# Kernel optimization log

Hardware: AMD Instinct MI355X
Metric: run time of the kernel (lower is better)

## Reference

```python
import jax, jax.numpy as jnp
import numpy as np

B, S, D = 4, 2048, 1024
NH = 16
H2 = NH // 2
F = D // NH  # per-head hidden = 64
EXP = 4
DECAY_CONST = S // 512  # 4
EPS = 1e-5


def setup_inputs() -> dict:
    key = jax.random.key(0)
    ks = jax.random.split(key, 8)
    inp = {
        "x": jax.random.normal(ks[0], (B, S, D), dtype=jnp.float32),
        # token_norm / channel_norm params (LayerNorm init: ones/zeros)
        "g1": jnp.ones((D,), jnp.float32), "b1": jnp.zeros((D,), jnp.float32),
        "g2": jnp.ones((D,), jnp.float32), "b2": jnp.zeros((D,), jnp.float32),
        # per-head input projections [NH, D, F] and output projection
        "Wp": jax.random.normal(ks[1], (NH, D, F), jnp.float32) * 0.02,
        "bp": jnp.zeros((NH, F), jnp.float32),
        "Wo": jax.random.normal(ks[2], (D, D), jnp.float32) * 0.02,
        "bo": jnp.zeros((D,), jnp.float32),
        # ColRepeatCausalLinear: weight = 0.4, bias = 3 ; RowRepeat: -0.3, 0.2
        "w_col": jnp.full((H2, S), 0.4, jnp.float32),
        "b_col": jnp.full((H2, S), 3.0, jnp.float32),
        "w_row": jnp.full((H2, S), -0.3, jnp.float32),
        "b_row": jnp.full((H2, S), 0.2, jnp.float32),
        # decay_value params (ones, clipped to [0.9, 1] then ** (1/decay_constant))
        "dcol": jnp.ones((H2,), jnp.float32),
        "drow": jnp.ones((H2,), jnp.float32),
        # channel MLP
        "W1": jax.random.normal(ks[3], (D, EXP * D), jnp.float32) * 0.02,
        "c1": jnp.zeros((EXP * D,), jnp.float32),
        "W2": jax.random.normal(ks[4], (EXP * D, D), jnp.float32) * 0.02,
        "c2": jnp.zeros((D,), jnp.float32),
    }
    return inp


def _ln(x, g, b):
    m = jnp.mean(x, axis=-1, keepdims=True)
    v = jnp.mean(jnp.square(x - m), axis=-1, keepdims=True)
    return (x - m) * jax.lax.rsqrt(v + EPS) * g + b


def _forward(x, g1, b1, g2, b2, Wp, bp, Wo, bo, w_col, b_col, w_row, b_row,
             dcol, drow, W1, c1, W2, c2):
    decay_c = jnp.clip(dcol, 0.9, 1.0) ** (1.0 / DECAY_CONST)  # [H2]
    decay_r = jnp.clip(drow, 0.9, 1.0) ** (1.0 / DECAY_CONST)  # [H2]

    def step(carry, inp):
        cc, rc = carry                      # each [B, H2, F]
        xt, wc, bc, wr, br = inp            # xt [B, D]; wc/bc/wr/br [H2]
        # token mixing branch
        h = _ln(xt, g1, b1)
        proj = jnp.einsum('bd,hdf->bhf', h, Wp) + bp  # [B, NH, F]
        # Col heads: cache = proj + decay*cache ; out = w*cache + b
        cc = proj[:, :H2] + decay_c[None, :, None] * cc
        col_out = wc[None, :, None] * cc + bc[None, :, None]
        # Row heads: cache = w*proj + decay*cache ; out = cache + b
        rc = wr[None, :, None] * proj[:, H2:] + decay_r[None, :, None] * rc
        row_out = rc + br[None, :, None]
        mix = jnp.concatenate([col_out, row_out], axis=1).reshape(xt.shape[0], -1)
        y = xt + mix @ Wo + bo
        # channel MLP branch
        h2 = _ln(y, g2, b2)
        out = y + jax.nn.gelu(h2 @ W1 + c1) @ W2 + c2
        return (cc, rc), out

    init = (jnp.zeros((x.shape[0], H2, F), x.dtype),
            jnp.zeros((x.shape[0], H2, F), x.dtype))
    xs = (jnp.swapaxes(x, 0, 1), w_col.T, b_col.T, w_row.T, b_row.T)
    _, ys = jax.lax.scan(step, init, xs)    # ys [S, B, D]
    return jnp.swapaxes(ys, 0, 1)


def reference(x, g1, b1, g2, b2, Wp, bp, Wo, bo, w_col, b_col, w_row, b_row,
              dcol, drow, W1, c1, W2, c2):
    return _forward(x, g1, b1, g2, b2, Wp, bp, Wo, bo, w_col, b_col,
                    w_row, b_row, dcol, drow, W1, c1, W2, c2)
```

## Files before the change

### kernel.cpp

```cpp
#include <hip/hip_runtime.h>

typedef __attribute__((ext_vector_type(4))) float fx4;
typedef __attribute__((ext_vector_type(8))) short s16x8;

#define SEQ   2048
#define DM    1024
#define BSZ   4
#define ROWS  (BSZ*SEQ)
#define CHUNK 64
#define NCH   (SEQ/CHUNK)

__device__ __forceinline__ unsigned short f2bf(float f){
  unsigned u = __builtin_bit_cast(unsigned, f);
  u = u + 0x7FFFu + ((u >> 16) & 1u);
  return (unsigned short)(u >> 16);
}

__device__ __forceinline__ float gelu_f(float x){
  float u = 0.7978845608028654f * (x + 0.044715f * x*x*x);
  return x / (1.0f + __expf(-2.0f*u));
}

__device__ __forceinline__ void gload_lds16(const void* g, void* l){
  __builtin_amdgcn_global_load_lds(
      (__attribute__((address_space(1))) void*)g,
      (__attribute__((address_space(3))) void*)l, 16, 0, 0);
}

__global__ __launch_bounds__(256) void transpose_k(const float* __restrict__ in,
    unsigned short* __restrict__ out, int R, int C, long long ibs, long long obs){
  __shared__ float tile[32][33];
  in  += (long long)blockIdx.z * ibs;
  out += (long long)blockIdx.z * obs;
  int c0 = blockIdx.x*32, r0 = blockIdx.y*32;
  int tx = threadIdx.x, ty = threadIdx.y;
  #pragma unroll
  for (int i=0;i<4;i++)
    tile[ty+8*i][tx] = in[(long long)(r0+ty+8*i)*C + c0+tx];
  __syncthreads();
  #pragma unroll
  for (int i=0;i<4;i++)
    out[(long long)(c0+ty+8*i)*R + r0+tx] = f2bf(tile[tx][ty+8*i]);
}

__global__ __launch_bounds__(256) void ln_rows(const float* __restrict__ x,
    const float* __restrict__ g, const float* __restrict__ b,
    unsigned short* __restrict__ out){
  int row = blockIdx.x, t = threadIdx.x;
  const fx4* xr = (const fx4*)(x + (long long)row*DM);
  fx4 v = xr[t];
  float s  = v[0]+v[1]+v[2]+v[3];
  float s2 = v[0]*v[0]+v[1]*v[1]+v[2]*v[2]+v[3]*v[3];
  #pragma unroll
  for (int o=32;o;o>>=1){ s += __shfl_down(s,o); s2 += __shfl_down(s2,o); }
  __shared__ float red[8];
  int lane = t & 63, wid = t >> 6;
  if (lane==0){ red[wid]=s; red[4+wid]=s2; }
  __syncthreads();
  s  = red[0]+red[1]+red[2]+red[3];
  s2 = red[4]+red[5]+red[6]+red[7];
  float m  = s * (1.0f/DM);
  float rs = rsqrtf(s2*(1.0f/DM) - m*m + 1e-5f);
  const fx4 gv = ((const fx4*)g)[t], bv = ((const fx4*)b)[t];
  ushort4 pk;
  pk.x = f2bf((v[0]-m)*rs*gv[0] + bv[0]);
  pk.y = f2bf((v[1]-m)*rs*gv[1] + bv[1]);
  pk.z = f2bf((v[2]-m)*rs*gv[2] + bv[2]);
  pk.w = f2bf((v[3]-m)*rs*gv[3] + bv[3]);
  *(ushort4*)(out + (long long)row*DM + t*4) = pk;
}

__global__ __launch_bounds__(256) void scan_carry(const float* __restrict__ P,
    const float* __restrict__ w_row, const float* __restrict__ dcol,
    const float* __restrict__ drow, float* __restrict__ carry){
  int g = blockIdx.x*4 + (threadIdx.x>>6);
  int lane = threadIdx.x & 63;
  int chunk = g & (NCH-1); int bh = g >> 5; int h = bh & 15; int b = bh >> 4;
  float draw = (h<8) ? dcol[h] : drow[h-8];
  float d = powf(fminf(fmaxf(draw,0.9f),1.0f), 0.25f);
  float c = 0.f;
  const float* p = P + ((long long)(b*SEQ + chunk*CHUNK))*DM + h*64 + lane;
  const float* wr = w_row + (h>=8 ? (h-8)*SEQ + chunk*CHUNK : 0);
  #pragma unroll 4
  for (int i=0;i<CHUNK;i++){
    float a = p[(long long)i*DM];
    if (h>=8) a *= wr[i];
    c = fmaf(d, c, a);
  }
  carry[((long long)(bh*64 + lane))*NCH + chunk] = c;
}

__global__ __launch_bounds__(256) void scan_final(const float* __restrict__ P,
    const float* __restrict__ w_col, const float* __restrict__ b_col,
    const float* __restrict__ w_row, const float* __restrict__ b_row,
    const float* __restrict__ dcol, const float* __restrict__ drow,
    const float* __restrict__ carry, unsigned short* __restrict__ mix){
  int g = blockIdx.x*4 + (threadIdx.x>>6);
  int lane = threadIdx.x & 63;
  int chunk = g & (NCH-1); int bh = g >> 5; int h = bh & 15; int b = bh >> 4;
  float draw = (h<8) ? dcol[h] : drow[h-8];
  float d = powf(fminf(fmaxf(draw,0.9f),1.0f), 0.25f);
  float dL = d;
  #pragma unroll
  for (int i=0;i<6;i++) dL *= dL;
  const float* cr = carry + ((long long)(bh*64 + lane))*NCH;
  float c = 0.f;
  for (int j=0;j<chunk;j++) c = fmaf(dL, c, cr[j]);
  const float* p = P + ((long long)(b*SEQ + chunk*CHUNK))*DM + h*64 + lane;
  unsigned short* mo = mix + ((long long)(b*SEQ + chunk*CHUNK))*DM + h*64 + lane;
  int t0 = chunk*CHUNK;
  #pragma unroll 4
  for (int i=0;i<CHUNK;i++){
    int t = t0 + i;
    float a = p[(long long)i*DM];
    float o;
    if (h<8){
      c = fmaf(d, c, a);
      o = w_col[h*SEQ + t]*c + b_col[h*SEQ + t];
    } else {
      a *= w_row[(h-8)*SEQ + t];
      c = fmaf(d, c, a);
      o = c + b_row[(h-8)*SEQ + t];
    }
    mo[(long long)i*DM] = f2bf(o);
  }
}

template<int EPI, int K>
__global__ __launch_bounds__(256) void gemm_bt(const unsigned short* __restrict__ A,
    const unsigned short* __restrict__ Bt, int N,
    const float* __restrict__ bias, const float* __restrict__ res,
    float* __restrict__ outf, unsigned short* __restrict__ outb){
  __shared__ __align__(16) unsigned short lds[32768];
  const int tid = threadIdx.x;
  const int l = tid & 63;
  const int w = tid >> 6;
  const int wr = w >> 1, wc = w & 1;

  const long long row0 = (long long)blockIdx.x * 128;
  const long long col0 = (long long)blockIdx.y * 128;

  fx4 acc[4][4] = {};

  const unsigned short* gA[4];
  const unsigned short* gB[4];
  int lslot[4];
  #pragma unroll
  for (int i=0;i<4;i++){
    int slot = w*256 + i*64 + l;
    int r = slot >> 3;
    int qs = slot & 7;
    int c = (qs ^ (r & 7)) << 3;
    gA[i] = A  + (row0 + r)*(long long)K + c;
    gB[i] = Bt + (col0 + r)*(long long)K + c;
    lslot[i] = slot*8;
  }
  int aoff[2][4], boff[2][4];
  #pragma unroll
  for (int kk=0;kk<2;kk++){
    #pragma unroll
    for (int m=0;m<4;m++){
      int r  = wr*64 + m*16 + (l&15);
      int q  = (kk*4 + (l>>4)) ^ (r&7);
      aoff[kk][m] = r*64 + q*8;
      int r2 = wc*64 + m*16 + (l&15);
      int q2 = (kk*4 + (l>>4)) ^ (r2&7);
      boff[kk][m] = 8192 + r2*64 + q2*8;
    }
  }

  constexpr int nsteps = K >> 6;

  #pragma unroll
  for (int i=0;i<4;i++){
    gload_lds16(gA[i], &lds[lslot[i]]);
    gload_lds16(gB[i], &lds[8192 + lslot[i]]);
    gA[i] += 64; gB[i] += 64;
  }
  __syncthreads();

  int curoff = 0;
  for (int s = 0; s < nsteps-1; ++s){
    int nxt = curoff ^ 16384;
    #pragma unroll
    for (int i=0;i<4;i++){
      gload_lds16(gA[i], &lds[nxt + lslot[i]]);
      gload_lds16(gB[i], &lds[nxt + 8192 + lslot[i]]);
      gA[i] += 64; gB[i] += 64;
    }
    __builtin_amdgcn_s_setprio(1);
    #pragma unroll
    for (int kk=0;kk<2;kk++){
      s16x8 af[4], bfr[4];
      #pragma unroll
      for (int m=0;m<4;m++) af[m]  = *(const s16x8*)&lds[curoff + aoff[kk][m]];
      #pragma unroll
      for (int n=0;n<4;n++) bfr[n] = *(const s16x8*)&lds[curoff + boff[kk][n]];
      #pragma unroll
      for (int m=0;m<4;m++)
        #pragma unroll
        for (int n=0;n<4;n++)
          acc[m][n] = __builtin_amdgcn_mfma_f32_16x16x32_bf16(af[m], bfr[n], acc[m][n], 0, 0, 0);
    }
    __builtin_amdgcn_s_setprio(0);
    __syncthreads();
    curoff = nxt;
  }
  __builtin_amdgcn_s_setprio(1);
  #pragma unroll
  for (int kk=0;kk<2;kk++){
    s16x8 af[4], bfr[4];
    #pragma unroll
    for (int m=0;m<4;m++) af[m]  = *(const s16x8*)&lds[curoff + aoff[kk][m]];
    #pragma unroll
    for (int n=0;n<4;n++) bfr[n] = *(const s16x8*)&lds[curoff + boff[kk][n]];
    #pragma unroll
    for (int m=0;m<4;m++)
      #pragma unroll
      for (int n=0;n<4;n++)
        acc[m][n] = __builtin_amdgcn_mfma_f32_16x16x32_bf16(af[m], bfr[n], acc[m][n], 0, 0, 0);
  }
  __builtin_amdgcn_s_setprio(0);
  __syncthreads();

  float* lf = (float*)lds;
  const int lg = l >> 4, lc = l & 15;
  #pragma unroll
  for (int g=0; g<4; ++g){
    if (wr == (g>>1)){
      #pragma unroll
      for (int mm=0; mm<2; ++mm){
        const int m = (g&1)*2 + mm;
        int lrow = mm*16 + lg*4;
        #pragma unroll
        for (int n=0;n<4;n++){
          int col = wc*64 + n*16 + lc;
          #pragma unroll
          for (int rg=0;rg<4;rg++)
            lf[(lrow+rg)*132 + col] = acc[m][n][rg];
        }
      }
    }
    __syncthreads();
    #pragma unroll
    for (int j=0;j<4;j++){
      int flat = j*256 + tid;
      int lrow = flat >> 5, c4 = flat & 31;
      long long grow = row0 + g*32 + lrow;
      long long gcol = col0 + c4*4;
      fx4 v = *(fx4*)&lf[lrow*132 + c4*4];
      fx4 bv = *(const fx4*)&bias[gcol];
      v = v + bv;
      long long idx = grow*(long long)N + gcol;
      if constexpr (EPI==0){
        *(fx4*)&outf[idx] = v;
      } else if constexpr (EPI==1){
        fx4 rv = *(const fx4*)&res[idx];
        v = v + rv;
        *(fx4*)&outf[idx] = v;
      } else {
        ushort4 pk;
        pk.x = f2bf(gelu_f(v[0]));
        pk.y = f2bf(gelu_f(v[1]));
        pk.z = f2bf(gelu_f(v[2]));
        pk.w = f2bf(gelu_f(v[3]));
        *(ushort4*)&outb[idx] = pk;
      }
    }
    __syncthreads();
  }
}

extern "C" void kernel_launch(void* const* d_in, const int* in_sizes, int n_in,
                              void* d_out, int out_size, void* d_ws, size_t ws_size,
                              hipStream_t stream){
  const float* x    = (const float*)d_in[0];
  const float* g1   = (const float*)d_in[1];
  const float* b1   = (const float*)d_in[2];
  const float* g2   = (const float*)d_in[3];
  const float* b2   = (const float*)d_in[4];
  const float* Wp   = (const float*)d_in[5];
  const float* bp   = (const float*)d_in[6];
  const float* Wo   = (const float*)d_in[7];
  const float* bo   = (const float*)d_in[8];
  const float* w_col= (const float*)d_in[9];
  const float* b_col= (const float*)d_in[10];
  const float* w_row= (const float*)d_in[11];
  const float* b_row= (const float*)d_in[12];
  const float* dcol = (const float*)d_in[13];
  const float* drow = (const float*)d_in[14];
  const float* W1   = (const float*)d_in[15];
  const float* c1   = (const float*)d_in[16];
  const float* W2   = (const float*)d_in[17];
  const float* c2   = (const float*)d_in[18];
  float* out = (float*)d_out;

  char* ws = (char*)d_ws;
  const size_t MB = 1024*1024;
  if (ws_size < 101*MB) return;
  unsigned short* Wpt = (unsigned short*)(ws + 0);
  unsigned short* Wot = (unsigned short*)(ws + 2*MB);
  unsigned short* W1t = (unsigned short*)(ws + 4*MB);
  unsigned short* W2t = (unsigned short*)(ws + 12*MB);
  unsigned short* h   = (unsigned short*)(ws + 20*MB);
  float*          P   = (float*)(ws + 36*MB);
  unsigned short* mix = (unsigned short*)(ws + 68*MB);
  float*          carry=(float*)(ws + 84*MB);
  unsigned short* U   = (unsigned short*)(ws + 36*MB);
  unsigned short* yln = h;

  dim3 tb(32,8);
  transpose_k<<<dim3(2,32,16),  tb, 0, stream>>>(Wp, Wpt, 1024,   64, 65536LL, 65536LL);
  transpose_k<<<dim3(32,32,1),  tb, 0, stream>>>(Wo, Wot, 1024, 1024, 0LL, 0LL);
  transpose_k<<<dim3(128,32,1), tb, 0, stream>>>(W1, W1t, 1024, 4096, 0LL, 0LL);
  transpose_k<<<dim3(32,128,1), tb, 0, stream>>>(W2, W2t, 4096, 1024, 0LL, 0LL);

  ln_rows<<<dim3(ROWS), dim3(256), 0, stream>>>(x, g1, b1, h);
  gemm_bt<0,1024><<<dim3(64,8),  dim3(256), 0, stream>>>(h,   Wpt, 1024, bp, nullptr, P, nullptr);
  scan_carry<<<dim3(512), dim3(256), 0, stream>>>(P, w_row, dcol, drow, carry);
  scan_final<<<dim3(512), dim3(256), 0, stream>>>(P, w_col, b_col, w_row, b_row, dcol, drow, carry, mix);
  gemm_bt<1,1024><<<dim3(64,8),  dim3(256), 0, stream>>>(mix, Wot, 1024, bo, x, out, nullptr);
  ln_rows<<<dim3(ROWS), dim3(256), 0, stream>>>(out, g2, b2, yln);
  gemm_bt<2,1024><<<dim3(64,32), dim3(256), 0, stream>>>(yln, W1t, 4096, c1, nullptr, nullptr, U);
  gemm_bt<1,4096><<<dim3(64,8),  dim3(256), 0, stream>>>(U,   W2t, 1024, c2, out, out, nullptr);
}
```

Measured before the change: 308.4 us.

## Deepen GEMM LDS prefetch pipeline and store projection output as bf16

```diff
diff --git a/kernel.cpp b/kernel.cpp
--- a/kernel.cpp
+++ b/kernel.cpp
@@ -14,6 +14,9 @@
   unsigned u = __builtin_bit_cast(unsigned, f);
   u = u + 0x7FFFu + ((u >> 16) & 1u);
   return (unsigned short)(u >> 16);
+}
+__device__ __forceinline__ float bf2f(unsigned short u){
+  return __builtin_bit_cast(float, ((unsigned)u) << 16);
 }
 
 __device__ __forceinline__ float gelu_f(float x){
@@ -70,7 +73,7 @@
   *(ushort4*)(out + (long long)row*DM + t*4) = pk;
 }
 
-__global__ __launch_bounds__(256) void scan_carry(const float* __restrict__ P,
+__global__ __launch_bounds__(256) void scan_carry(const unsigned short* __restrict__ P,
     const float* __restrict__ w_row, const float* __restrict__ dcol,
     const float* __restrict__ drow, float* __restrict__ carry){
   int g = blockIdx.x*4 + (threadIdx.x>>6);
@@ -79,18 +82,18 @@
   float draw = (h<8) ? dcol[h] : drow[h-8];
   float d = powf(fminf(fmaxf(draw,0.9f),1.0f), 0.25f);
   float c = 0.f;
-  const float* p = P + ((long long)(b*SEQ + chunk*CHUNK))*DM + h*64 + lane;
+  const unsigned short* p = P + ((long long)(b*SEQ + chunk*CHUNK))*DM + h*64 + lane;
   const float* wr = w_row + (h>=8 ? (h-8)*SEQ + chunk*CHUNK : 0);
   #pragma unroll 4
   for (int i=0;i<CHUNK;i++){
-    float a = p[(long long)i*DM];
+    float a = bf2f(p[(long long)i*DM]);
     if (h>=8) a *= wr[i];
     c = fmaf(d, c, a);
   }
   carry[((long long)(bh*64 + lane))*NCH + chunk] = c;
 }
 
-__global__ __launch_bounds__(256) void scan_final(const float* __restrict__ P,
+__global__ __launch_bounds__(256) void scan_final(const unsigned short* __restrict__ P,
     const float* __restrict__ w_col, const float* __restrict__ b_col,
     const float* __restrict__ w_row, const float* __restrict__ b_row,
     const float* __restrict__ dcol, const float* __restrict__ drow,
@@ -106,13 +109,13 @@
   const float* cr = carry + ((long long)(bh*64 + lane))*NCH;
   float c = 0.f;
   for (int j=0;j<chunk;j++) c = fmaf(dL, c, cr[j]);
-  const float* p = P + ((long long)(b*SEQ + chunk*CHUNK))*DM + h*64 + lane;
+  const unsigned short* p = P + ((long long)(b*SEQ + chunk*CHUNK))*DM + h*64 + lane;
   unsigned short* mo = mix + ((long long)(b*SEQ + chunk*CHUNK))*DM + h*64 + lane;
   int t0 = chunk*CHUNK;
   #pragma unroll 4
   for (int i=0;i<CHUNK;i++){
     int t = t0 + i;
-    float a = p[(long long)i*DM];
+    float a = bf2f(p[(long long)i*DM]);
     float o;
     if (h<8){
       c = fmaf(d, c, a);
@@ -169,58 +172,60 @@
     }
   }
 
+  auto STAGE = [&](int bufoff){
+    #pragma unroll
+    for (int i=0;i<4;i++){
+      gload_lds16(gA[i], &lds[bufoff + lslot[i]]);
+      gload_lds16(gB[i], &lds[bufoff + 8192 + lslot[i]]);
+      gA[i] += 64; gB[i] += 64;
+    }
+  };
+
   constexpr int nsteps = K >> 6;
 
-  #pragma unroll
-  for (int i=0;i<4;i++){
-    gload_lds16(gA[i], &lds[lslot[i]]);
-    gload_lds16(gB[i], &lds[8192 + lslot[i]]);
-    gA[i] += 64; gB[i] += 64;
-  }
-  __syncthreads();
+  STAGE(0);
+  STAGE(16384);
+  asm volatile("s_waitcnt vmcnt(8)" ::: "memory");
+  __builtin_amdgcn_sched_barrier(0);
+  __builtin_amdgcn_s_barrier();
 
   int curoff = 0;
-  for (int s = 0; s < nsteps-1; ++s){
-    int nxt = curoff ^ 16384;
-    #pragma unroll
-    for (int i=0;i<4;i++){
-      gload_lds16(gA[i], &lds[nxt + lslot[i]]);
-      gload_lds16(gB[i], &lds[nxt + 8192 + lslot[i]]);
-      gA[i] += 64; gB[i] += 64;
-    }
+  for (int s = 0; s < nsteps; ++s){
+    s16x8 af[2][4], bfr[2][4];
+    #pragma unroll
+    for (int kk=0;kk<2;kk++){
+      #pragma unroll
+      for (int m=0;m<4;m++){
+        af[kk][m]  = *(const s16x8*)&lds[curoff + aoff[kk][m]];
+        bfr[kk][m] = *(const s16x8*)&lds[curoff + boff[kk][m]];
+      }
+    }
+    __builtin_amdgcn_sched_barrier(0);
+    asm volatile("s_waitcnt lgkmcnt(0)" ::: "memory");
+    __builtin_amdgcn_sched_barrier(0);
+    __builtin_amdgcn_s_barrier();
+    __builtin_amdgcn_sched_barrier(0);
+    const bool do_stage = (s + 2 < nsteps);
+    if (do_stage) STAGE(curoff);
     __builtin_amdgcn_s_setprio(1);
     #pragma unroll
-    for (int kk=0;kk<2;kk++){
-      s16x8 af[4], bfr[4];
-      #pragma unroll
-      for (int m=0;m<4;m++) af[m]  = *(const s16x8*)&lds[curoff + aoff[kk][m]];
-      #pragma unroll
-      for (int n=0;n<4;n++) bfr[n] = *(const s16x8*)&lds[curoff + boff[kk][n]];
+    for (int kk=0;kk<2;kk++)
       #pragma unroll
       for (int m=0;m<4;m++)
         #pragma unroll
         for (int n=0;n<4;n++)
-          acc[m][n] = __builtin_amdgcn_mfma_f32_16x16x32_bf16(af[m], bfr[n], acc[m][n], 0, 0, 0);
-    }
+          acc[m][n] = __builtin_amdgcn_mfma_f32_16x16x32_bf16(af[kk][m], bfr[kk][n], acc[m][n], 0, 0, 0);
     __builtin_amdgcn_s_setprio(0);
-    __syncthreads();
-    curoff = nxt;
-  }
-  __builtin_amdgcn_s_setprio(1);
-  #pragma unroll
-  for (int kk=0;kk<2;kk++){
-    s16x8 af[4], bfr[4];
-    #pragma unroll
-    for (int m=0;m<4;m++) af[m]  = *(const s16x8*)&lds[curoff + aoff[kk][m]];
-    #pragma unroll
-    for (int n=0;n<4;n++) bfr[n] = *(const s16x8*)&lds[curoff + boff[kk][n]];
-    #pragma unroll
-    for (int m=0;m<4;m++)
-      #pragma unroll
-      for (int n=0;n<4;n++)
-        acc[m][n] = __builtin_amdgcn_mfma_f32_16x16x32_bf16(af[m], bfr[n], acc[m][n], 0, 0, 0);
-  }
-  __builtin_amdgcn_s_setprio(0);
+    if (s + 1 < nsteps){
+      __builtin_amdgcn_sched_barrier(0);
+      if (do_stage) asm volatile("s_waitcnt vmcnt(8)" ::: "memory");
+      else          asm volatile("s_waitcnt vmcnt(0)" ::: "memory");
+      __builtin_amdgcn_sched_barrier(0);
+      __builtin_amdgcn_s_barrier();
+      __builtin_amdgcn_sched_barrier(0);
+    }
+    curoff ^= 16384;
+  }
   __syncthreads();
 
   float* lf = (float*)lds;
@@ -258,12 +263,17 @@
         fx4 rv = *(const fx4*)&res[idx];
         v = v + rv;
         *(fx4*)&outf[idx] = v;
-      } else {
+      } else if constexpr (EPI==2){
         ushort4 pk;
         pk.x = f2bf(gelu_f(v[0]));
         pk.y = f2bf(gelu_f(v[1]));
         pk.z = f2bf(gelu_f(v[2]));
         pk.w = f2bf(gelu_f(v[3]));
+        *(ushort4*)&outb[idx] = pk;
+      } else {
+        ushort4 pk;
+        pk.x = f2bf(v[0]); pk.y = f2bf(v[1]);
+        pk.z = f2bf(v[2]); pk.w = f2bf(v[3]);
         *(ushort4*)&outb[idx] = pk;
       }
     }
@@ -303,7 +313,7 @@
   unsigned short* W1t = (unsigned short*)(ws + 4*MB);
   unsigned short* W2t = (unsigned short*)(ws + 12*MB);
   unsigned short* h   = (unsigned short*)(ws + 20*MB);
-  float*          P   = (float*)(ws + 36*MB);
+  unsigned short* P   = (unsigned short*)(ws + 36*MB);
   unsigned short* mix = (unsigned short*)(ws + 68*MB);
   float*          carry=(float*)(ws + 84*MB);
   unsigned short* U   = (unsigned short*)(ws + 36*MB);
@@ -316,7 +326,7 @@
   transpose_k<<<dim3(32,128,1), tb, 0, stream>>>(W2, W2t, 4096, 1024, 0LL, 0LL);
 
   ln_rows<<<dim3(ROWS), dim3(256), 0, stream>>>(x, g1, b1, h);
-  gemm_bt<0,1024><<<dim3(64,8),  dim3(256), 0, stream>>>(h,   Wpt, 1024, bp, nullptr, P, nullptr);
+  gemm_bt<3,1024><<<dim3(64,8),  dim3(256), 0, stream>>>(h,   Wpt, 1024, bp, nullptr, nullptr, P);
   scan_carry<<<dim3(512), dim3(256), 0, stream>>>(P, w_row, dcol, drow, carry);
   scan_final<<<dim3(512), dim3(256), 0, stream>>>(P, w_col, b_col, w_row, b_row, dcol, drow, carry, mix);
   gemm_bt<1,1024><<<dim3(64,8),  dim3(256), 0, stream>>>(mix, Wot, 1024, bo, x, out, nullptr);
```

Result: no change. 311.7 us (+1.1%).
